# Performance work log

Hardware: AMD Instinct MI355X
Metric: run time of the kernel (lower is better)

## Reference

```python
import jax, jax.numpy as jnp
import numpy as np
import math

B, S, D, H = 4, 2048, 1024, 16
HD = D // H  # head_dim = 64


def _rope_tables(max_len, half_dim, theta=10000.0):
    inv_freq = 1.0 / (theta ** (jnp.arange(0, half_dim, dtype=jnp.float32) / half_dim))
    ang = jnp.arange(max_len, dtype=jnp.float32)[:, None] * inv_freq[None, :]  # [max_len, half_dim]
    return jnp.cos(ang), jnp.sin(ang)


def _apply_rope(x, cos, sin):
    # x: [B, H, S, HD]; cos/sin: [S, HD/2]
    x1, x2 = x[..., ::2], x[..., 1::2]
    # matches torch.cat([x1*cos - x2*sin, x1*sin + x2*cos], dim=-1)
    return jnp.concatenate([x1 * cos - x2 * sin, x1 * sin + x2 * cos], axis=-1)


def setup_inputs() -> dict:
    key = jax.random.key(0)
    kx, kq, ko = jax.random.split(key, 3)
    x = jax.random.normal(kx, (B, S, D), dtype=jnp.float32)
    Wqkv = jax.random.normal(kq, (D, 3 * D), dtype=jnp.float32) / math.sqrt(D)
    Wout = jax.random.normal(ko, (D, D), dtype=jnp.float32) / math.sqrt(D)
    cos, sin = _rope_tables(S, HD // 2)
    # causal additive mask, per-batch as in module signature [B, S, S]
    causal = jnp.where(jnp.tril(jnp.ones((S, S), dtype=bool)), 0.0, -1e9).astype(jnp.float32)
    mask = jnp.broadcast_to(causal, (B, S, S))
    return {"x": x, "cos": cos, "sin": sin, "mask": mask, "Wqkv": Wqkv, "Wout": Wout}


def reference(x, cos, sin, mask, Wqkv, Wout):
    b, s, d = x.shape
    qkv = x @ Wqkv  # [B, S, 3D]
    q, k, v = jnp.split(qkv, 3, axis=-1)
    def to_heads(t):
        return t.reshape(b, s, H, HD).transpose(0, 2, 1, 3)  # [B, H, S, HD]
    q, k, v = to_heads(q), to_heads(k), to_heads(v)
    q = _apply_rope(q, cos[:s], sin[:s])
    k = _apply_rope(k, cos[:s], sin[:s])
    scores = jnp.einsum("bhqd,bhkd->bhqk", q, k) / math.sqrt(HD)
    attn = jax.nn.softmax(scores + mask[:, None, :, :], axis=-1)
    out = jnp.einsum("bhqk,bhkd->bhqd", attn, v)  # [B, H, S, HD]
    out = out.transpose(0, 2, 1, 3).reshape(b, s, d)
    return out @ Wout
```

## Files before the change

### kernel.cpp

```cpp
#include <hip/hip_runtime.h>
#include <hip/hip_bf16.h>
#include <stdint.h>

#define B_   4
#define S_   2048
#define D_   1024
#define H_   16
#define HD_  64
#define BH_  (B_*H_)
#define MROWS (B_*S_)

typedef short  short8  __attribute__((ext_vector_type(8)));
typedef float  floatx4 __attribute__((ext_vector_type(4)));

__device__ __forceinline__ ushort f2bf(float f) {
    union { float f; uint32_t u; } v; v.f = f;
    uint32_t u = v.u;
    return (ushort)((u + 0x7FFFu + ((u >> 16) & 1u)) >> 16);
}
__device__ __forceinline__ float bf2f(ushort b) {
    union { uint32_t u; float f; } v; v.u = ((uint32_t)b) << 16;
    return v.f;
}
__device__ __forceinline__ float u2f(uint32_t u) {
    union { uint32_t u; float f; } v; v.u = u; return v.f;
}
__device__ __forceinline__ uint32_t f2u(float f) {
    union { float f; uint32_t u; } v; v.f = f; return v.u;
}

__device__ __forceinline__ void gl_lds16(const ushort* g, ushort* l) {
    __builtin_amdgcn_global_load_lds(
        (const __attribute__((address_space(1))) unsigned int*)g,
        (__attribute__((address_space(3))) unsigned int*)l,
        16, 0, 0);
}

__global__ void k_f32_to_bf16(const float* __restrict__ in, ushort* __restrict__ out, int n) {
    int i = (blockIdx.x * blockDim.x + threadIdx.x) * 4;
    if (i + 3 < n) {
        float4 f = *(const float4*)(in + i);
        ushort4 o; o.x = f2bf(f.x); o.y = f2bf(f.y); o.z = f2bf(f.z); o.w = f2bf(f.w);
        *(ushort4*)(out + i) = o;
    }
}

__global__ void k_transpose_to_bf16(const float* __restrict__ in, ushort* __restrict__ out,
                                    int R, int C) {
    __shared__ float tile[32][33];
    int bx = blockIdx.x * 32;
    int by = blockIdx.y * 32;
    int tx = threadIdx.x;
    int ty = threadIdx.y;
    #pragma unroll
    for (int j = 0; j < 32; j += 8)
        tile[ty + j][tx] = in[(size_t)(by + ty + j) * C + bx + tx];
    __syncthreads();
    #pragma unroll
    for (int j = 0; j < 32; j += 8)
        out[(size_t)(bx + ty + j) * R + by + tx] = f2bf(tile[tx][ty + j]);
}

__global__ void k_vtrans(const ushort* __restrict__ Vb, ushort* __restrict__ VbT) {
    __shared__ __align__(16) ushort t[64 * 72];
    int bh = blockIdx.x >> 5;
    int s0 = (blockIdx.x & 31) * 64;
    int tid = threadIdx.x;
    int ss = tid >> 2, c0 = (tid & 3) * 16;
    size_t base = (size_t)bh * S_ * HD_;
    *(uint4*)&t[ss * 72 + c0]     = *(const uint4*)&Vb[base + (size_t)(s0 + ss) * HD_ + c0];
    *(uint4*)&t[ss * 72 + c0 + 8] = *(const uint4*)&Vb[base + (size_t)(s0 + ss) * HD_ + c0 + 8];
    __syncthreads();
    int hd = tid >> 2, q0 = (tid & 3) * 16;
    ushort tmp[16];
    #pragma unroll
    for (int e = 0; e < 16; e++) tmp[e] = t[(q0 + e) * 72 + hd];
    size_t obase = (size_t)bh * HD_ * S_ + (size_t)hd * S_ + s0 + q0;
    *(uint4*)&VbT[obase]     = *(const uint4*)&tmp[0];
    *(uint4*)&VbT[obase + 8] = *(const uint4*)&tmp[8];
}

#define BM 128
#define BN 128
#define BK 32
#define LDT 32

template<int EPI>
__global__ __launch_bounds__(256)
void k_gemm(const ushort* __restrict__ A, const ushort* __restrict__ Bt,
            float* __restrict__ outF,
            ushort* __restrict__ q_out, ushort* __restrict__ k_out, ushort* __restrict__ v_out,
            int M, int N, int K) {
    __shared__ __align__(16) ushort As[BM * LDT];
    __shared__ __align__(16) ushort Bs[BN * LDT];
    int tid  = threadIdx.x;
    int lane = tid & 63;
    int wave = tid >> 6;
    int quad = lane >> 4;
    int l16  = lane & 15;
    int bm = blockIdx.y * BM;
    int bn = blockIdx.x * BN;
    int wm = (wave >> 1) * 64;
    int wn = (wave & 1) * 64;

    floatx4 acc[4][4] = {};

    for (int k0 = 0; k0 < K; k0 += BK) {
        __syncthreads();
        #pragma unroll
        for (int p = 0; p < 2; p++) {
            int c   = p * 256 + tid;
            int row = c >> 2;
            int kc  = (c & 3) << 3;
            gl_lds16(&A[(size_t)(bm + row) * K + k0 + kc],  &As[c * 8]);
            gl_lds16(&Bt[(size_t)(bn + row) * K + k0 + kc], &Bs[c * 8]);
        }
        __syncthreads();
        short8 af[4], bf[4];
        #pragma unroll
        for (int mt = 0; mt < 4; mt++)
            af[mt] = *(const short8*)&As[(wm + mt * 16 + l16) * LDT + quad * 8];
        #pragma unroll
        for (int nt = 0; nt < 4; nt++)
            bf[nt] = *(const short8*)&Bs[(wn + nt * 16 + l16) * LDT + quad * 8];
        #pragma unroll
        for (int mt = 0; mt < 4; mt++)
            #pragma unroll
            for (int nt = 0; nt < 4; nt++)
                acc[mt][nt] = __builtin_amdgcn_mfma_f32_16x16x32_bf16(af[mt], bf[nt], acc[mt][nt], 0, 0, 0);
    }

    #pragma unroll
    for (int mt = 0; mt < 4; mt++)
        #pragma unroll
        for (int nt = 0; nt < 4; nt++)
            #pragma unroll
            for (int r = 0; r < 4; r++) {
                int row = bm + wm + mt * 16 + quad * 4 + r;
                int col = bn + wn + nt * 16 + l16;
                float v = acc[mt][nt][r];
                if (EPI == 0) {
                    int which = col >> 10;
                    int rem   = col & 1023;
                    int h  = rem >> 6, hd = rem & 63;
                    int b  = row >> 11, s  = row & 2047;
                    size_t idx = ((size_t)(b * H_ + h) * S_ + s) * HD_ + hd;
                    ushort bv = f2bf(v);
                    ushort* dst = (which == 0) ? q_out : (which == 1) ? k_out : v_out;
                    dst[idx] = bv;
                } else {
                    outF[(size_t)row * N + col] = v;
                }
            }
}

__global__ void k_rope(ushort* __restrict__ Q, ushort* __restrict__ Kv,
                       const float* __restrict__ cosT, const float* __restrict__ sinT) {
    int wid  = (blockIdx.x * 256 + threadIdx.x) >> 6;
    int lane = threadIdx.x & 63;
    int s  = wid & (S_ - 1);
    int bh = wid >> 11;
    int i  = lane & 31;
    float c  = cosT[s * 32 + i];
    float sn = sinT[s * 32 + i];
    size_t base = ((size_t)bh * S_ + s) * HD_;

    uint32_t uq = *(const uint32_t*)&Q[base + 2 * i];
    float x1 = u2f(uq << 16), x2 = u2f(uq & 0xFFFF0000u);
    float o  = (lane < 32) ? (x1 * c - x2 * sn) : (x1 * sn + x2 * c);
    Q[base + lane] = f2bf(o * 0.125f);

    uint32_t uk = *(const uint32_t*)&Kv[base + 2 * i];
    x1 = u2f(uk << 16); x2 = u2f(uk & 0xFFFF0000u);
    o  = (lane < 32) ? (x1 * c - x2 * sn) : (x1 * sn + x2 * c);
    Kv[base + lane] = f2bf(o);
}

__global__ __launch_bounds__(256, 4)
void k_attn(const ushort* __restrict__ Q, const ushort* __restrict__ K,
            const ushort* __restrict__ VT, ushort* __restrict__ O) {
    __shared__ __align__(16) ushort Ksp[2][64 * 32];
    __shared__ __align__(16) ushort Vtp[2][64 * 32];
    __shared__ __align__(16) ushort Pst[4][32 * 72];
    __shared__ float Lw[4][32];

    int tid  = threadIdx.x;
    int lane = tid & 63;
    int wave = tid >> 6;
    int quad = lane >> 4;
    int l16  = lane & 15;

    int bh   = blockIdx.x & 63;
    int qblk = 15 - (blockIdx.x >> 6);
    int qb0  = qblk * 128;
    size_t hbase = (size_t)bh * S_ * HD_;
    size_t vbase = (size_t)bh * HD_ * S_;

    int mrow[2] = { qb0 + wave * 16, qb0 + 64 + wave * 16 };

    short8 qf[2][2];
    #pragma unroll
    for (int m = 0; m < 2; m++)
        #pragma unroll
        for (int h = 0; h < 2; h++)
            qf[m][h] = *(const short8*)&Q[hbase + (size_t)(mrow[m] + l16) * HD_ + quad * 8 + h * 32];

    floatx4 acc[2][4] = {};
    float lsum[2] = {0.0f, 0.0f};

    int crow = tid >> 2;
    int coff = (tid & 3) * 8;

    int nk = 2 * qblk + 2;
    for (int kb = 0; kb < nk; kb++) {
        int k0 = kb * 64;
        __syncthreads();
        #pragma unroll
        for (int h = 0; h < 2; h++)
            gl_lds16(&K[hbase + (size_t)(k0 + crow) * HD_ + h * 32 + coff], &Ksp[h][tid * 8]);
        #pragma unroll
        for (int k2 = 0; k2 < 2; k2++)
            gl_lds16(&VT[vbase + (size_t)crow * S_ + k0 + k2 * 32 + coff], &Vtp[k2][tid * 8]);
        __syncthreads();

        bool act[2] = { k0 <= mrow[0] + 15, k0 <= mrow[1] + 15 };

        short8 kf[4][2];
        #pragma unroll
        for (int kt = 0; kt < 4; kt++)
            #pragma unroll
            for (int h = 0; h < 2; h++)
                kf[kt][h] = *(const short8*)&Ksp[h][(kt * 16 + l16) * 32 + quad * 8];

        #pragma unroll
        for (int m = 0; m < 2; m++) {
            if (!act[m]) continue;
            floatx4 sc[4] = {};
            #pragma unroll
            for (int kt = 0; kt < 4; kt++)
                #pragma unroll
                for (int h = 0; h < 2; h++)
                    sc[kt] = __builtin_amdgcn_mfma_f32_16x16x32_bf16(kf[kt][h], qf[m][h], sc[kt], 0, 0, 0);
            bool needMask = (k0 + 63 > mrow[m]);
            int qr = mrow[m] + l16;
            #pragma unroll
            for (int kt = 0; kt < 4; kt++) {
                float p[4];
                #pragma unroll
                for (int r = 0; r < 4; r++) {
                    float v = __expf(sc[kt][r]);
                    if (needMask) {
                        int kc = k0 + kt * 16 + quad * 4 + r;
                        if (kc > qr) v = 0.0f;
                    }
                    p[r] = v;
                }
                lsum[m] += (p[0] + p[1]) + (p[2] + p[3]);
                uint2 pk;
                pk.x = __builtin_amdgcn_perm(f2u(p[1]) + 0x8000u, f2u(p[0]) + 0x8000u, 0x07060302u);
                pk.y = __builtin_amdgcn_perm(f2u(p[3]) + 0x8000u, f2u(p[2]) + 0x8000u, 0x07060302u);
                *(uint2*)&Pst[wave][(m * 16 + l16) * 72 + kt * 16 + quad * 4] = pk;
            }
        }

        #pragma unroll
        for (int k2 = 0; k2 < 2; k2++) {
            short8 vb[4];
            #pragma unroll
            for (int nt = 0; nt < 4; nt++)
                vb[nt] = *(const short8*)&Vtp[k2][(nt * 16 + l16) * 32 + quad * 8];
            #pragma unroll
            for (int m = 0; m < 2; m++) {
                if (!act[m]) continue;
                short8 pa = *(const short8*)&Pst[wave][(m * 16 + l16) * 72 + k2 * 32 + quad * 8];
                #pragma unroll
                for (int nt = 0; nt < 4; nt++)
                    acc[m][nt] = __builtin_amdgcn_mfma_f32_16x16x32_bf16(pa, vb[nt], acc[m][nt], 0, 0, 0);
            }
        }
    }

    #pragma unroll
    for (int m = 0; m < 2; m++) {
        lsum[m] += __shfl_xor(lsum[m], 16);
        lsum[m] += __shfl_xor(lsum[m], 32);
        if (quad == 0) Lw[wave][m * 16 + l16] = lsum[m];
    }

    int b = bh >> 4, h = bh & 15;
    #pragma unroll
    for (int m = 0; m < 2; m++)
        #pragma unroll
        for (int r = 0; r < 4; r++) {
            float inv = 1.0f / Lw[wave][m * 16 + quad * 4 + r];
            int qr = mrow[m] + quad * 4 + r;
            #pragma unroll
            for (int nt = 0; nt < 4; nt++)
                O[((size_t)(b * S_ + qr)) * D_ + h * HD_ + nt * 16 + l16] = f2bf(acc[m][nt][r] * inv);
        }
}

extern "C" void kernel_launch(void* const* d_in, const int* in_sizes, int n_in,
                              void* d_out, int out_size, void* d_ws, size_t ws_size,
                              hipStream_t stream) {
    const float* x    = (const float*)d_in[0];
    const float* cosT = (const float*)d_in[1];
    const float* sinT = (const float*)d_in[2];
    const float* Wqkv = (const float*)d_in[4];
    const float* Wout = (const float*)d_in[5];
    float* out = (float*)d_out;

    ushort* ws = (ushort*)d_ws;
    ushort* Xbf    = ws;
    ushort* WqkvT  = Xbf    + (size_t)MROWS * D_;
    ushort* WoutT  = WqkvT  + (size_t)3 * D_ * D_;
    ushort* Qb     = WoutT  + (size_t)D_ * D_;
    ushort* Kb     = Qb     + (size_t)BH_ * S_ * HD_;
    ushort* Vb     = Kb     + (size_t)BH_ * S_ * HD_;
    ushort* VbT    = Vb     + (size_t)BH_ * S_ * HD_;
    ushort* AO     = Xbf;

    k_f32_to_bf16<<<(MROWS * D_) / 1024, 256, 0, stream>>>(x, Xbf, MROWS * D_);
    k_transpose_to_bf16<<<dim3(3 * D_ / 32, D_ / 32), dim3(32, 8), 0, stream>>>(Wqkv, WqkvT, D_, 3 * D_);
    k_transpose_to_bf16<<<dim3(D_ / 32, D_ / 32), dim3(32, 8), 0, stream>>>(Wout, WoutT, D_, D_);
    k_gemm<0><<<dim3(3 * D_ / BN, MROWS / BM), 256, 0, stream>>>(Xbf, WqkvT, nullptr, Qb, Kb, Vb,
                                                                 MROWS, 3 * D_, D_);
    k_rope<<<(BH_ * S_ * 64) / 256, 256, 0, stream>>>(Qb, Kb, cosT, sinT);
    k_vtrans<<<BH_ * 32, 256, 0, stream>>>(Vb, VbT);
    k_attn<<<1024, 256, 0, stream>>>(Qb, Kb, VbT, AO);
    k_gemm<1><<<dim3(D_ / BN, MROWS / BM), 256, 0, stream>>>(AO, WoutT, out, nullptr, nullptr, nullptr,
                                                             MROWS, D_, D_);
}
```

Measured before the change: 346.0 us.

## Compute softmax row sums via MFMA with ones vector and use exp2

Moves the softmax denominator from per-lane scalar adds plus shuffle reduction and LDS staging into an extra MFMA that multiplies the bf16 P tile by a vector of ones, so the sum arrives in the accumulator layout directly. Folds log2(e) into the Q scaling so exp2f replaces __expf. Also loads K and V fragments from LDS just before each MFMA instead of preloading them into registers, to reduce register pressure. The row sum now comes from bf16-rounded probabilities, which slightly changes numerics but stays consistent with the P used for PV.

After: 333.7 us. -3.6%, faster.

```diff
diff --git a/kernel.cpp b/kernel.cpp
--- a/kernel.cpp
+++ b/kernel.cpp
@@ -17,10 +17,6 @@
     union { float f; uint32_t u; } v; v.f = f;
     uint32_t u = v.u;
     return (ushort)((u + 0x7FFFu + ((u >> 16) & 1u)) >> 16);
-}
-__device__ __forceinline__ float bf2f(ushort b) {
-    union { uint32_t u; float f; } v; v.u = ((uint32_t)b) << 16;
-    return v.f;
 }
 __device__ __forceinline__ float u2f(uint32_t u) {
     union { uint32_t u; float f; } v; v.u = u; return v.f;
@@ -168,7 +164,7 @@
     uint32_t uq = *(const uint32_t*)&Q[base + 2 * i];
     float x1 = u2f(uq << 16), x2 = u2f(uq & 0xFFFF0000u);
     float o  = (lane < 32) ? (x1 * c - x2 * sn) : (x1 * sn + x2 * c);
-    Q[base + lane] = f2bf(o * 0.125f);
+    Q[base + lane] = f2bf(o * 0.1803368801f);
 
     uint32_t uk = *(const uint32_t*)&Kv[base + 2 * i];
     x1 = u2f(uk << 16); x2 = u2f(uk & 0xFFFF0000u);
@@ -182,7 +178,6 @@
     __shared__ __align__(16) ushort Ksp[2][64 * 32];
     __shared__ __align__(16) ushort Vtp[2][64 * 32];
     __shared__ __align__(16) ushort Pst[4][32 * 72];
-    __shared__ float Lw[4][32];
 
     int tid  = threadIdx.x;
     int lane = tid & 63;
@@ -205,8 +200,12 @@
         for (int h = 0; h < 2; h++)
             qf[m][h] = *(const short8*)&Q[hbase + (size_t)(mrow[m] + l16) * HD_ + quad * 8 + h * 32];
 
+    short8 ones;
+    #pragma unroll
+    for (int e = 0; e < 8; e++) ones[e] = (short)0x3F80;
+
     floatx4 acc[2][4] = {};
-    float lsum[2] = {0.0f, 0.0f};
+    floatx4 accl[2] = {};
 
     int crow = tid >> 2;
     int coff = (tid & 3) * 8;
@@ -225,13 +224,6 @@
 
         bool act[2] = { k0 <= mrow[0] + 15, k0 <= mrow[1] + 15 };
 
-        short8 kf[4][2];
-        #pragma unroll
-        for (int kt = 0; kt < 4; kt++)
-            #pragma unroll
-            for (int h = 0; h < 2; h++)
-                kf[kt][h] = *(const short8*)&Ksp[h][(kt * 16 + l16) * 32 + quad * 8];
-
         #pragma unroll
         for (int m = 0; m < 2; m++) {
             if (!act[m]) continue;
@@ -239,8 +231,10 @@
             #pragma unroll
             for (int kt = 0; kt < 4; kt++)
                 #pragma unroll
-                for (int h = 0; h < 2; h++)
-                    sc[kt] = __builtin_amdgcn_mfma_f32_16x16x32_bf16(kf[kt][h], qf[m][h], sc[kt], 0, 0, 0);
+                for (int h = 0; h < 2; h++) {
+                    short8 kf = *(const short8*)&Ksp[h][(kt * 16 + l16) * 32 + quad * 8];
+                    sc[kt] = __builtin_amdgcn_mfma_f32_16x16x32_bf16(kf, qf[m][h], sc[kt], 0, 0, 0);
+                }
             bool needMask = (k0 + 63 > mrow[m]);
             int qr = mrow[m] + l16;
             #pragma unroll
@@ -248,14 +242,13 @@
                 float p[4];
                 #pragma unroll
                 for (int r = 0; r < 4; r++) {
-                    float v = __expf(sc[kt][r]);
+                    float v = exp2f(sc[kt][r]);
                     if (needMask) {
                         int kc = k0 + kt * 16 + quad * 4 + r;
                         if (kc > qr) v = 0.0f;
                     }
                     p[r] = v;
                 }
-                lsum[m] += (p[0] + p[1]) + (p[2] + p[3]);
                 uint2 pk;
                 pk.x = __builtin_amdgcn_perm(f2u(p[1]) + 0x8000u, f2u(p[0]) + 0x8000u, 0x07060302u);
                 pk.y = __builtin_amdgcn_perm(f2u(p[3]) + 0x8000u, f2u(p[2]) + 0x8000u, 0x07060302u);
@@ -265,34 +258,26 @@
 
         #pragma unroll
         for (int k2 = 0; k2 < 2; k2++) {
-            short8 vb[4];
-            #pragma unroll
-            for (int nt = 0; nt < 4; nt++)
-                vb[nt] = *(const short8*)&Vtp[k2][(nt * 16 + l16) * 32 + quad * 8];
             #pragma unroll
             for (int m = 0; m < 2; m++) {
                 if (!act[m]) continue;
                 short8 pa = *(const short8*)&Pst[wave][(m * 16 + l16) * 72 + k2 * 32 + quad * 8];
                 #pragma unroll
-                for (int nt = 0; nt < 4; nt++)
-                    acc[m][nt] = __builtin_amdgcn_mfma_f32_16x16x32_bf16(pa, vb[nt], acc[m][nt], 0, 0, 0);
+                for (int nt = 0; nt < 4; nt++) {
+                    short8 vb = *(const short8*)&Vtp[k2][(nt * 16 + l16) * 32 + quad * 8];
+                    acc[m][nt] = __builtin_amdgcn_mfma_f32_16x16x32_bf16(pa, vb, acc[m][nt], 0, 0, 0);
+                }
+                accl[m] = __builtin_amdgcn_mfma_f32_16x16x32_bf16(pa, ones, accl[m], 0, 0, 0);
             }
         }
     }
 
-    #pragma unroll
-    for (int m = 0; m < 2; m++) {
-        lsum[m] += __shfl_xor(lsum[m], 16);
-        lsum[m] += __shfl_xor(lsum[m], 32);
-        if (quad == 0) Lw[wave][m * 16 + l16] = lsum[m];
-    }
-
     int b = bh >> 4, h = bh & 15;
     #pragma unroll
     for (int m = 0; m < 2; m++)
         #pragma unroll
         for (int r = 0; r < 4; r++) {
-            float inv = 1.0f / Lw[wave][m * 16 + quad * 4 + r];
+            float inv = 1.0f / accl[m][r];
             int qr = mrow[m] + quad * 4 + r;
             #pragma unroll
             for (int nt = 0; nt < 4; nt++)
```
